# Optimization experiments

Hardware: AMD Instinct MI355X
Metric: run time of the kernel (lower is better)

The kernel has to match this reference:

```python
import jax, jax.numpy as jnp
import numpy as np


def _scattering(image, mags, phases):
    # image: [B,S,S] real; mags/phases: [J,L,S,S] real (Fourier-domain Morlet filters)
    J = mags.shape[0]
    psi = (mags * jnp.exp(1j * phases)).astype(jnp.complex64)        # [J,L,S,S]
    xf = jnp.fft.fft2(image)                                          # [B,S,S] complex64
    # first-order: modulus of wavelet convolutions, all scales/orientations at once
    u1 = jnp.abs(jnp.fft.ifft2(xf[:, None, None] * psi[None]))        # [B,J,L,S,S]
    s0 = image.mean(axis=(-2, -1))                                    # [B]
    s1 = u1.mean(axis=(2, 3, 4))                                      # [B,J] (orientation-averaged)
    # second-order: only j2 > j1 (the nan-filtered entries in the original)
    s2_parts = []
    for j1 in range(J - 1):  # structural loop over scales, not data dims
        u1f = jnp.fft.fft2(u1[:, j1].astype(jnp.complex64))           # [B,L1,S,S]
        psi2 = psi[j1 + 1:]                                           # [J2,L2,S,S]
        v = jnp.abs(jnp.fft.ifft2(u1f[:, :, None, None] * psi2[None, None]))  # [B,L1,J2,L2,S,S]
        s2_parts.append(v.mean(axis=(1, 3, 4, 5)))                    # [B,J2]
    s2 = jnp.concatenate(s2_parts, axis=1)                            # [B, J*(J-1)/2]
    return s0, s1, s2


def setup_inputs() -> dict:
    key = jax.random.key(0)
    ks = jax.random.split(key, 8)
    B, S, J, L = 64, 128, 6, 4
    return {
        "image_batch": jax.random.normal(ks[0], (B, S, S), dtype=jnp.float32),
        "mags": jax.random.uniform(ks[1], (J, L, S, S), dtype=jnp.float32),
        "phases": jax.random.normal(ks[2], (J, L, S, S), dtype=jnp.float32),
        "w1": jax.random.normal(ks[3], (22, 16), dtype=jnp.float32) * 0.1,
        "b1": jnp.zeros((16,), dtype=jnp.float32),
        "w2": jax.random.normal(ks[4], (16, 16), dtype=jnp.float32) * 0.1,
        "b2": jnp.zeros((16,), dtype=jnp.float32),
        "w3": jax.random.normal(ks[5], (16, 1), dtype=jnp.float32) * 0.1,
        "b3": jnp.zeros((1,), dtype=jnp.float32),
    }


def reference(image_batch, mags, phases, w1, b1, w2, b2, w3, b3):
    s0, s1, s2 = _scattering(image_batch, mags, phases)
    x = jnp.concatenate([s0[:, None], s1, s2], axis=1)                # [B,22]
    x = jax.nn.relu(x @ w1 + b1)
    x = jax.nn.relu(x @ w2 + b2)
    x = jax.nn.sigmoid(x @ w3 + b3)
    return jnp.squeeze(x, axis=1)                                     # [B]
```

## Files before the change

kernel.cpp:

```cpp
#include <hip/hip_runtime.h>
#include <math.h>


#define SDIM 128
#define PLANE 16384
#define PITCH 129
#define NT 1024
#define TWO_PI 6.28318530717958647692f

constexpr float W16R[8] = {1.f, 0.9238795325f, 0.7071067812f, 0.3826834324f,
                           0.f, -0.3826834324f, -0.7071067812f, -0.9238795325f};
constexpr float W16I[8] = {0.f, -0.3826834324f, -0.7071067812f, -0.9238795325f,
                           -1.f, -0.9238795325f, -0.7071067812f, -0.3826834324f};

__device__ __forceinline__ float fast_sqrtf(float x) {
  return __builtin_amdgcn_sqrtf(x);
}

__device__ __forceinline__ unsigned packbf(float re, float im) {
  const unsigned r = __float_as_uint(re) + 0x8000u;
  const unsigned i = __float_as_uint(im) + 0x8000u;
  return __builtin_amdgcn_perm(r, i, 0x07060302u);
}
__device__ __forceinline__ void unpackbf(unsigned u, float& re, float& im) {
  re = __uint_as_float(u & 0xFFFF0000u);
  im = __uint_as_float(u << 16);
}

__device__ __forceinline__ void stC(float2* s, int idx, float re, float im) { s[idx] = make_float2(re, im); }
__device__ __forceinline__ void ldC(const float2* s, int idx, float& re, float& im) { const float2 v = s[idx]; re = v.x; im = v.y; }
__device__ __forceinline__ void stC(unsigned* s, int idx, float re, float im) { s[idx] = packbf(re, im); }
__device__ __forceinline__ void ldC(const unsigned* s, int idx, float& re, float& im) { unpackbf(s[idx], re, im); }

__device__ __forceinline__ void load_tw(const float2* __restrict__ twg, int g,
                                        float* twr, float* twi) {
#pragma unroll
  for (int k = 1; k < 16; ++k) {
    const float2 w = twg[16 * g + k];
    twr[k] = __uint_as_float(__builtin_amdgcn_readfirstlane(__float_as_uint(w.x)));
    twi[k] = __uint_as_float(__builtin_amdgcn_readfirstlane(__float_as_uint(w.y)));
  }
}

template<bool INV>
__device__ __forceinline__ void bfly(float& ar, float& ai, float& br, float& bi, const int idx) {
  float tr, ti;
  if (idx == 0) {
    tr = br; ti = bi;
  } else if (idx == 4) {
    if (INV) { tr = -bi; ti = br; } else { tr = bi; ti = -br; }
  } else {
    const float wr = W16R[idx];
    const float wi = INV ? -W16I[idx] : W16I[idx];
    tr = br * wr - bi * wi;
    ti = br * wi + bi * wr;
  }
  br = ar - tr; bi = ai - ti;
  ar = ar + tr; ai = ai + ti;
}

#define CSWAP(re, im, a, b) { float _t = re[a]; re[a]=re[b]; re[b]=_t; _t = im[a]; im[a]=im[b]; im[b]=_t; }

template<bool INV>
__device__ __forceinline__ void dft16(float* re, float* im) {
  CSWAP(re, im, 1, 8) CSWAP(re, im, 2, 4) CSWAP(re, im, 3, 12)
  CSWAP(re, im, 5, 10) CSWAP(re, im, 7, 14) CSWAP(re, im, 11, 13)
#pragma unroll
  for (int ls = 1; ls <= 4; ++ls) {
    const int len = 1 << ls, half = len >> 1, tstep = 16 >> ls;
#pragma unroll
    for (int blk = 0; blk < 16; blk += len)
#pragma unroll
      for (int j = 0; j < half; ++j)
        bfly<INV>(re[blk + j], im[blk + j], re[blk + j + half], im[blk + j + half], j * tstep);
  }
}

template<bool INV>
__device__ __forceinline__ void dft8(float* re, float* im) {
  CSWAP(re, im, 1, 4) CSWAP(re, im, 3, 6)
#pragma unroll
  for (int ls = 1; ls <= 3; ++ls) {
    const int len = 1 << ls, half = len >> 1, tstep = 8 >> ls;
#pragma unroll
    for (int blk = 0; blk < 8; blk += len)
#pragma unroll
      for (int j = 0; j < half; ++j)
        bfly<INV>(re[blk + j], im[blk + j], re[blk + j + half], im[blk + j + half], j * tstep * 2);
  }
}

__device__ __forceinline__ void twmul_fwd(float* R, float* I, const float* twr, const float* twi) {
#pragma unroll
  for (int k = 1; k < 16; ++k) {
    const float r = R[k] * twr[k] - I[k] * twi[k];
    I[k] = R[k] * twi[k] + I[k] * twr[k]; R[k] = r;
  }
}
__device__ __forceinline__ void twmul_inv(float* R, float* I, const float* twr, const float* twi) {
#pragma unroll
  for (int k = 1; k < 16; ++k) {
    const float r = R[k] * twr[k] + I[k] * twi[k];
    I[k] = I[k] * twr[k] - R[k] * twi[k]; R[k] = r;
  }
}

template<typename S>
__device__ __forceinline__ void fwd_fft2(float* R, float* I, S* sC,
                                         int g, int q, const float* twr, const float* twi) {
  const int rb = q * PITCH;
  dft16<false>(R, I);
  twmul_fwd(R, I, twr, twi);
  __syncthreads();
#pragma unroll
  for (int k = 0; k < 16; ++k) stC(sC, rb + 8 * k + g, R[k], I[k]);
  __syncthreads();
#pragma unroll
  for (int t = 0; t < 8; ++t) {
    ldC(sC, rb + 16 * g + t, R[t], I[t]);
    ldC(sC, rb + 16 * g + 8 + t, R[8 + t], I[8 + t]);
  }
  dft8<false>(R, I); dft8<false>(R + 8, I + 8);
#pragma unroll
  for (int k2 = 0; k2 < 8; ++k2) {
    stC(sC, rb + 16 * g + k2, R[k2], I[k2]);
    stC(sC, rb + 16 * g + 8 + k2, R[8 + k2], I[8 + k2]);
  }
  __syncthreads();
#pragma unroll
  for (int m = 0; m < 16; ++m) ldC(sC, (g + 8 * m) * PITCH + q, R[m], I[m]);
  dft16<false>(R, I);
  twmul_fwd(R, I, twr, twi);
#pragma unroll
  for (int k = 0; k < 16; ++k) stC(sC, (8 * k + g) * PITCH + q, R[k], I[k]);
  __syncthreads();
#pragma unroll
  for (int u = 0; u < 8; ++u) {
    const int bp = (16 * g + 2 * u) * PITCH + q;
    ldC(sC, bp, R[2 * u], I[2 * u]);
    ldC(sC, bp + PITCH, R[2 * u + 1], I[2 * u + 1]);
  }
  dft8<false>(R, I); dft8<false>(R + 8, I + 8);
}

template<bool FIRST, typename S>
__device__ __forceinline__ void inv_fft2(float* R, float* I, S* sC,
                                         int g, int q, const float* twr, const float* twi) {
  const int rb = q * PITCH;
  dft8<true>(R, I); dft8<true>(R + 8, I + 8);
  if constexpr (!FIRST) __syncthreads();
#pragma unroll
  for (int t = 0; t < 16; ++t) stC(sC, rb + 16 * g + t, R[t], I[t]);
  __syncthreads();
#pragma unroll
  for (int k = 0; k < 16; ++k) ldC(sC, rb + 8 * k + g, R[k], I[k]);
  twmul_inv(R, I, twr, twi);
  dft16<true>(R, I);
#pragma unroll
  for (int m = 0; m < 16; ++m) stC(sC, rb + g + 8 * m, R[m], I[m]);
  __syncthreads();
#pragma unroll
  for (int u = 0; u < 8; ++u) {
    const int bp = (16 * g + 2 * u) * PITCH + q;
    ldC(sC, bp, R[2 * u], I[2 * u]);
    ldC(sC, bp + PITCH, R[2 * u + 1], I[2 * u + 1]);
  }
  dft8<true>(R, I); dft8<true>(R + 8, I + 8);
#pragma unroll
  for (int u = 0; u < 8; ++u) {
    const int bp = (16 * g + 2 * u) * PITCH + q;
    stC(sC, bp, R[2 * u], I[2 * u]);
    stC(sC, bp + PITCH, R[2 * u + 1], I[2 * u + 1]);
  }
  __syncthreads();
#pragma unroll
  for (int k = 0; k < 16; ++k) ldC(sC, (8 * k + g) * PITCH + q, R[k], I[k]);
  twmul_inv(R, I, twr, twi);
  dft16<true>(R, I);
}

__device__ __forceinline__ float block_reduce_sum(float v, float* red, int tid) {
#pragma unroll
  for (int o = 32; o > 0; o >>= 1) v += __shfl_down(v, o);
  __syncthreads();
  if ((tid & 63) == 0) red[tid >> 6] = v;
  __syncthreads();
  float t = 0.0f;
  if (tid == 0) {
#pragma unroll
    for (int w = 0; w < 16; ++w) t += red[w];
  }
  return t;
}

__global__ __launch_bounds__(256) void k_psi(const float* __restrict__ mags,
                                             const float* __restrict__ phases,
                                             float2* __restrict__ psi,
                                             float2* __restrict__ twg) {
  if (blockIdx.x == 0 && threadIdx.x < 128) {
    const int gg = threadIdx.x >> 4, k = threadIdx.x & 15;
    float sn, cs;
    __sincosf(-TWO_PI * (float)(gg * k) * (1.0f / 128.0f), &sn, &cs);
    twg[threadIdx.x] = make_float2(cs, sn);
  }
  const int gid = blockIdx.x * 256 + threadIdx.x;
  const int p = gid >> 14;
  const int rem = gid & (PLANE - 1);
  const int e = rem & 1;
  const int tt = (rem >> 1) & 1023;
  const int i = rem >> 11;
  const int j = 2 * i + e;
  const int g = tt >> 7, q = tt & 127;
  const int pr = 16 * g + j, pc = q;
  const int kr = (pr >> 3) + 16 * (pr & 7);
  const int kc = (pc >> 3) + 16 * (pc & 7);
  const int src = (p << 14) + kr * SDIM + kc;
  const float m = mags[src] * (1.0f / 16384.0f);
  float sn, cs;
  __sincosf(phases[src], &sn, &cs);
  psi[gid] = make_float2(m * cs, m * sn);
}

__global__ __launch_bounds__(NT) void k_img_fft(const float* __restrict__ img,
                                                float2* __restrict__ Xf,
                                                float* __restrict__ s0,
                                                const float2* __restrict__ twg) {
  __shared__ float2 sC[SDIM * PITCH];
  __shared__ float red[16];
  const int tid = threadIdx.x, b = blockIdx.x;
  const int g = __builtin_amdgcn_readfirstlane(tid >> 7);
  const int q = tid & 127;
  float twr[16], twi[16];
  load_tw(twg, g, twr, twi);
  const float* ip = img + b * PLANE;
  float sum = 0.0f;
#pragma unroll
  for (int kk = 0; kk < 16; ++kk) {
    const int e = tid + kk * NT;
    const float v = ip[e];
    sC[(e >> 7) * PITCH + (e & 127)] = make_float2(v, 0.0f);
    sum += v;
  }
  const float tot = block_reduce_sum(sum, red, tid);
  if (tid == 0) s0[b] = tot * (1.0f / 16384.0f);
  __syncthreads();
  float R[16], I[16];
#pragma unroll
  for (int m = 0; m < 16; ++m) { R[m] = sC[q * PITCH + g + 8 * m].x; I[m] = 0.0f; }
  fwd_fft2(R, I, sC, g, q, twr, twi);
  float4* x4 = (float4*)Xf + (size_t)b * 8192 + tid;
#pragma unroll
  for (int i = 0; i < 8; ++i)
    x4[i * 1024] = make_float4(R[2 * i], I[2 * i], R[2 * i + 1], I[2 * i + 1]);
}

__global__ __launch_bounds__(NT) void k_scat_a(const float2* __restrict__ Xf,
                                               const float2* __restrict__ psi,
                                               float* __restrict__ s1num,
                                               unsigned* __restrict__ Ubuf,
                                               const float2* __restrict__ twg) {
  __shared__ unsigned sU[SDIM * PITCH];
  __shared__ float red[16];
  const int tid = threadIdx.x;
  const int g = __builtin_amdgcn_readfirstlane(tid >> 7);
  const int q = tid & 127;
  float twr[16], twi[16];
  load_tw(twg, g, twr, twi);
  const int bid = blockIdx.x;
  float R[16], I[16];

  if (bid < 1280) {
    const int j1 = bid >> 8;
    const int b = (bid & 255) >> 2;
    const int l1 = bid & 3;
    const float4* x4 = (const float4*)Xf + (size_t)b * 8192 + tid;
    const float4* p4 = (const float4*)psi + (size_t)(j1 * 4 + l1) * 8192 + tid;
#pragma unroll
    for (int i = 0; i < 8; ++i) {
      const float4 x = x4[i * 1024], v = p4[i * 1024];
      R[2 * i]     = x.x * v.x - x.y * v.y;  I[2 * i]     = x.x * v.y + x.y * v.x;
      R[2 * i + 1] = x.z * v.z - x.w * v.w;  I[2 * i + 1] = x.z * v.w + x.w * v.z;
    }
    inv_fft2<true>(R, I, sU, g, q, twr, twi);
    float s1sum = 0.0f;
#pragma unroll
    for (int m = 0; m < 16; ++m) {
      const float a = fast_sqrtf(R[m] * R[m] + I[m] * I[m]);
      s1sum += a; R[m] = a; I[m] = 0.0f;
    }
    fwd_fft2(R, I, sU, g, q, twr, twi);
    uint4 ob[4];
    unsigned* obs = (unsigned*)ob;
#pragma unroll
    for (int j = 0; j < 16; ++j) obs[j] = packbf(R[j], I[j]);
    uint4* o4 = (uint4*)Ubuf + (size_t)((b * 5 + j1) * 4 + l1) * 4096 + tid;
#pragma unroll
    for (int i = 0; i < 4; ++i) o4[i * 1024] = ob[i];
    const float tot = block_reduce_sum(s1sum, red, tid);
    if (tid == 0) atomicAdd(&s1num[b * 6 + j1], tot);
  } else {
    const int idx = bid - 1280;
    const int b = idx >> 2, l = idx & 3;
    const float4* x4 = (const float4*)Xf + (size_t)b * 8192 + tid;
    const float4* p4 = (const float4*)psi + (size_t)(20 + l) * 8192 + tid;
#pragma unroll
    for (int i = 0; i < 8; ++i) {
      const float4 x = x4[i * 1024], v = p4[i * 1024];
      R[2 * i]     = x.x * v.x - x.y * v.y;  I[2 * i]     = x.x * v.y + x.y * v.x;
      R[2 * i + 1] = x.z * v.z - x.w * v.w;  I[2 * i + 1] = x.z * v.w + x.w * v.z;
    }
    inv_fft2<true>(R, I, sU, g, q, twr, twi);
    float s = 0.0f;
#pragma unroll
    for (int m = 0; m < 16; ++m) s += fast_sqrtf(R[m] * R[m] + I[m] * I[m]);
    const float tot = block_reduce_sum(s, red, tid);
    if (tid == 0) atomicAdd(&s1num[b * 6 + 5], tot);
  }
}

__global__ __launch_bounds__(NT) void k_scat_b(const float2* __restrict__ psi,
                                               const unsigned* __restrict__ Ubuf,
                                               float* __restrict__ s2num,
                                               const float2* __restrict__ twg) {
  __shared__ unsigned sU[SDIM * PITCH];
  __shared__ float red[16];
  const int tid = threadIdx.x;
  const int g = __builtin_amdgcn_readfirstlane(tid >> 7);
  const int q = tid & 127;
  float twr[16], twi[16];
  load_tw(twg, g, twr, twi);
  int t = blockIdx.x;
  const int l2 = t & 3; t >>= 2;
  const int pair = t % 15; t /= 15;
  const int l1 = t & 3;
  const int b = t >> 2;
  int j1 = 0, base = 0;
  if (pair >= 14)      { j1 = 4; base = 14; }
  else if (pair >= 12) { j1 = 3; base = 12; }
  else if (pair >= 9)  { j1 = 2; base = 9; }
  else if (pair >= 5)  { j1 = 1; base = 5; }
  const int j2 = j1 + 1 + (pair - base);
  float R[16], I[16];
  {
    const uint4* u4 = (const uint4*)Ubuf + (size_t)((b * 5 + j1) * 4 + l1) * 4096 + tid;
    uint4 ub[4];
#pragma unroll
    for (int i = 0; i < 4; ++i) ub[i] = u4[i * 1024];
    const unsigned* ubs = (const unsigned*)ub;
    const float4* p4 = (const float4*)psi + (size_t)(j2 * 4 + l2) * 8192 + tid;
#pragma unroll
    for (int i = 0; i < 8; ++i) {
      const float4 v = p4[i * 1024];
      float ur, ui;
      unpackbf(ubs[2 * i], ur, ui);
      R[2 * i] = ur * v.x - ui * v.y;      I[2 * i] = ur * v.y + ui * v.x;
      unpackbf(ubs[2 * i + 1], ur, ui);
      R[2 * i + 1] = ur * v.z - ui * v.w;  I[2 * i + 1] = ur * v.w + ui * v.z;
    }
  }
  inv_fft2<true>(R, I, sU, g, q, twr, twi);
  float vsum = 0.0f;
#pragma unroll
  for (int m = 0; m < 16; ++m) vsum += fast_sqrtf(R[m] * R[m] + I[m] * I[m]);
  const float tot = block_reduce_sum(vsum, red, tid);
  if (tid == 0) atomicAdd(&s2num[b * 15 + pair], tot);
}

__global__ __launch_bounds__(NT) void k_scat_mono(const float2* __restrict__ Xf,
                                                  const float2* __restrict__ psi,
                                                  float* __restrict__ s1num,
                                                  float* __restrict__ s2num,
                                                  const float2* __restrict__ twg) {
  __shared__ unsigned sU[SDIM * PITCH];
  __shared__ float red[16];
  const int tid = threadIdx.x;
  const int g = __builtin_amdgcn_readfirstlane(tid >> 7);
  const int q = tid & 127;
  float twr[16], twi[16];
  load_tw(twg, g, twr, twi);
  const int bid = blockIdx.x;
  float R[16], I[16];
  if (bid < 1280) {
    const int j1 = bid >> 8;
    const int b = (bid & 255) >> 2;
    const int l1 = bid & 3;
    const float4* x4 = (const float4*)Xf + (size_t)b * 8192 + tid;
    const float4* p4 = (const float4*)psi + (size_t)(j1 * 4 + l1) * 8192 + tid;
#pragma unroll
    for (int i = 0; i < 8; ++i) {
      const float4 x = x4[i * 1024], v = p4[i * 1024];
      R[2 * i]     = x.x * v.x - x.y * v.y;  I[2 * i]     = x.x * v.y + x.y * v.x;
      R[2 * i + 1] = x.z * v.z - x.w * v.w;  I[2 * i + 1] = x.z * v.w + x.w * v.z;
    }
    inv_fft2<true>(R, I, sU, g, q, twr, twi);
    float s1sum = 0.0f;
#pragma unroll
    for (int m = 0; m < 16; ++m) {
      const float a = fast_sqrtf(R[m] * R[m] + I[m] * I[m]);
      s1sum += a; R[m] = a; I[m] = 0.0f;
    }
    fwd_fft2(R, I, sU, g, q, twr, twi);
    float Ur[16], Ui[16];
#pragma unroll
    for (int k = 0; k < 16; ++k) { Ur[k] = R[k]; Ui[k] = I[k]; }
    {
      const float tot = block_reduce_sum(s1sum, red, tid);
      if (tid == 0) atomicAdd(&s1num[b * 6 + j1], tot);
    }
    const int pb = (j1 * (11 - j1)) >> 1;
    int plane = (j1 + 1) * 4;
#pragma unroll 1
    for (int j2 = j1 + 1; j2 <= 5; ++j2) {
      float vsum = 0.0f;
#pragma unroll 1
      for (int l2 = 0; l2 < 4; ++l2) {
        const float4* q4 = (const float4*)psi + (size_t)plane * 8192 + tid;
#pragma unroll
        for (int i = 0; i < 8; ++i) {
          const float4 v = q4[i * 1024];
          R[2 * i]     = Ur[2 * i] * v.x - Ui[2 * i] * v.y;
          I[2 * i]     = Ur[2 * i] * v.y + Ui[2 * i] * v.x;
          R[2 * i + 1] = Ur[2 * i + 1] * v.z - Ui[2 * i + 1] * v.w;
          I[2 * i + 1] = Ur[2 * i + 1] * v.w + Ui[2 * i + 1] * v.z;
        }
        inv_fft2<false>(R, I, sU, g, q, twr, twi);
#pragma unroll
        for (int m = 0; m < 16; ++m) vsum += fast_sqrtf(R[m] * R[m] + I[m] * I[m]);
        ++plane;
      }
      const float tot = block_reduce_sum(vsum, red, tid);
      if (tid == 0) atomicAdd(&s2num[b * 15 + pb + (j2 - j1 - 1)], tot);
    }
  } else {
    const int idx = bid - 1280;
    const int b = idx >> 2, l = idx & 3;
    const float4* x4 = (const float4*)Xf + (size_t)b * 8192 + tid;
    const float4* p4 = (const float4*)psi + (size_t)(20 + l) * 8192 + tid;
#pragma unroll
    for (int i = 0; i < 8; ++i) {
      const float4 x = x4[i * 1024], v = p4[i * 1024];
      R[2 * i]     = x.x * v.x - x.y * v.y;  I[2 * i]     = x.x * v.y + x.y * v.x;
      R[2 * i + 1] = x.z * v.z - x.w * v.w;  I[2 * i + 1] = x.z * v.w + x.w * v.z;
    }
    inv_fft2<true>(R, I, sU, g, q, twr, twi);
    float s = 0.0f;
#pragma unroll
    for (int m = 0; m < 16; ++m) s += fast_sqrtf(R[m] * R[m] + I[m] * I[m]);
    const float tot = block_reduce_sum(s, red, tid);
    if (tid == 0) atomicAdd(&s1num[b * 6 + 5], tot);
  }
}

__global__ __launch_bounds__(64) void k_final(const float* __restrict__ s0,
                                              const float* __restrict__ s1num,
                                              const float* __restrict__ s2num,
                                              const float* __restrict__ w1,
                                              const float* __restrict__ b1,
                                              const float* __restrict__ w2,
                                              const float* __restrict__ b2,
                                              const float* __restrict__ w3,
                                              const float* __restrict__ b3,
                                              float* __restrict__ out) {
  const int b = threadIdx.x;
  if (b >= 64) return;
  float x[22];
  x[0] = s0[b];
#pragma unroll
  for (int j = 0; j < 6; ++j) x[1 + j] = s1num[b * 6 + j] * (1.0f / (4.0f * 16384.0f));
#pragma unroll
  for (int p = 0; p < 15; ++p) x[7 + p] = s2num[b * 15 + p] * (1.0f / (16.0f * 16384.0f));
  float h1[16];
#pragma unroll
  for (int o = 0; o < 16; ++o) {
    float t = b1[o];
    for (int i = 0; i < 22; ++i) t += x[i] * w1[i * 16 + o];
    h1[o] = fmaxf(t, 0.0f);
  }
  float h2[16];
#pragma unroll
  for (int o = 0; o < 16; ++o) {
    float t = b2[o];
    for (int i = 0; i < 16; ++i) t += h1[i] * w2[i * 16 + o];
    h2[o] = fmaxf(t, 0.0f);
  }
  float t = b3[0];
#pragma unroll
  for (int i = 0; i < 16; ++i) t += h2[i] * w3[i];
  out[b] = 1.0f / (1.0f + expf(-t));
}

extern "C" void kernel_launch(void* const* d_in, const int* in_sizes, int n_in,
                              void* d_out, int out_size, void* d_ws, size_t ws_size,
                              hipStream_t stream) {
  (void)in_sizes; (void)n_in; (void)out_size;
  const float* image  = (const float*)d_in[0];
  const float* mags   = (const float*)d_in[1];
  const float* phases = (const float*)d_in[2];
  const float* w1 = (const float*)d_in[3];
  const float* b1 = (const float*)d_in[4];
  const float* w2 = (const float*)d_in[5];
  const float* b2 = (const float*)d_in[6];
  const float* w3 = (const float*)d_in[7];
  const float* b3 = (const float*)d_in[8];
  float* out = (float*)d_out;

  char* ws = (char*)d_ws;
  float2* psi = (float2*)ws;
  float2* Xf  = (float2*)(ws + 3145728);
  float*  s0  = (float*)(ws + 11534336);
  float*  s1n = s0 + 64;
  float*  s2n = s1n + 384;
  float2* twg = (float2*)(s2n + 960);
  unsigned* Ubuf = (unsigned*)(ws + 11542528);
  const size_t need = 11542528ull + 83886080ull;

  hipMemsetAsync(s1n, 0, (384 + 960) * sizeof(float), stream);
  k_psi<<<dim3(1536), dim3(256), 0, stream>>>(mags, phases, psi, twg);
  k_img_fft<<<dim3(64), dim3(NT), 0, stream>>>(image, Xf, s0, twg);
  if (ws_size >= need) {
    k_scat_a<<<dim3(1536), dim3(NT), 0, stream>>>(Xf, psi, s1n, Ubuf, twg);
    k_scat_b<<<dim3(15360), dim3(NT), 0, stream>>>(psi, Ubuf, s2n, twg);
  } else {
    k_scat_mono<<<dim3(1536), dim3(NT), 0, stream>>>(Xf, psi, s1n, s2n, twg);
  }
  k_final<<<dim3(1), dim3(64), 0, stream>>>(s0, s1n, s2n, w1, b1, w2, b2, w3, b3, out);
}
```

Before: 502.2 us.

## Restructure 2D FFT shared-memory layout to replace block barriers with wave-local fences

Remaps thread-to-data assignment (g = tid&7, q = tid>>3) so that each radix-16/8 sub-FFT exchange stays inside one wavefront. Several __syncthreads are replaced by s_waitcnt LDS fences, and a new blocked transpose layout (TBLK stride) leaves only one full barrier per transpose. Twiddles are cut to 9 entries, with factors 9..15 built by multiplying by w8, which lowers register pressure. The psi permutation and the launch bounds are updated to match. The intra-wave fences depend on lockstep wavefront execution, and the extra complex multiplies add ALU work.

```diff
diff --git a/kernel.cpp b/kernel.cpp
--- a/kernel.cpp
+++ b/kernel.cpp
@@ -4,8 +4,9 @@
 
 #define SDIM 128
 #define PLANE 16384
-#define PITCH 129
 #define NT 1024
+#define SSTR 136
+#define TBLK 1088
 #define TWO_PI 6.28318530717958647692f
 
 constexpr float W16R[8] = {1.f, 0.9238795325f, 0.7071067812f, 0.3826834324f,
@@ -17,6 +18,10 @@
   return __builtin_amdgcn_sqrtf(x);
 }
 
+__device__ __forceinline__ void ldsfence() {
+  asm volatile("s_waitcnt lgkmcnt(0)" ::: "memory");
+}
+
 __device__ __forceinline__ unsigned packbf(float re, float im) {
   const unsigned r = __float_as_uint(re) + 0x8000u;
   const unsigned i = __float_as_uint(im) + 0x8000u;
@@ -32,14 +37,22 @@
 __device__ __forceinline__ void stC(unsigned* s, int idx, float re, float im) { s[idx] = packbf(re, im); }
 __device__ __forceinline__ void ldC(const unsigned* s, int idx, float& re, float& im) { unpackbf(s[idx], re, im); }
 
-__device__ __forceinline__ void load_tw(const float2* __restrict__ twg, int g,
-                                        float* twr, float* twi) {
-#pragma unroll
-  for (int k = 1; k < 16; ++k) {
-    const float2 w = twg[16 * g + k];
-    twr[k] = __uint_as_float(__builtin_amdgcn_readfirstlane(__float_as_uint(w.x)));
-    twi[k] = __uint_as_float(__builtin_amdgcn_readfirstlane(__float_as_uint(w.y)));
-  }
+__device__ __forceinline__ void load_tw8(const float2* __restrict__ twg, int g,
+                                         float* twr, float* twi) {
+  const float4* t4 = (const float4*)(twg + 16 * g);
+  const float4 a = t4[0];
+  const float4 b = t4[1];
+  const float4 c = t4[2];
+  const float4 d = t4[3];
+  const float2 e8 = twg[16 * g + 8];
+  twr[1] = a.z; twi[1] = a.w;
+  twr[2] = b.x; twi[2] = b.y;
+  twr[3] = b.z; twi[3] = b.w;
+  twr[4] = c.x; twi[4] = c.y;
+  twr[5] = c.z; twi[5] = c.w;
+  twr[6] = d.x; twi[6] = d.y;
+  twr[7] = d.z; twi[7] = d.w;
+  twr[8] = e8.x; twi[8] = e8.y;
 }
 
 template<bool INV>
@@ -92,91 +105,125 @@
 
 __device__ __forceinline__ void twmul_fwd(float* R, float* I, const float* twr, const float* twi) {
 #pragma unroll
-  for (int k = 1; k < 16; ++k) {
+  for (int k = 1; k <= 8; ++k) {
     const float r = R[k] * twr[k] - I[k] * twi[k];
     I[k] = R[k] * twi[k] + I[k] * twr[k]; R[k] = r;
   }
+#pragma unroll
+  for (int k = 9; k < 16; ++k) {
+    const float r = R[k] * twr[k - 8] - I[k] * twi[k - 8];
+    const float i = R[k] * twi[k - 8] + I[k] * twr[k - 8];
+    R[k] = r * twr[8] - i * twi[8];
+    I[k] = r * twi[8] + i * twr[8];
+  }
 }
 __device__ __forceinline__ void twmul_inv(float* R, float* I, const float* twr, const float* twi) {
 #pragma unroll
-  for (int k = 1; k < 16; ++k) {
+  for (int k = 1; k <= 8; ++k) {
     const float r = R[k] * twr[k] + I[k] * twi[k];
     I[k] = I[k] * twr[k] - R[k] * twi[k]; R[k] = r;
   }
+#pragma unroll
+  for (int k = 9; k < 16; ++k) {
+    const float r = R[k] * twr[k - 8] + I[k] * twi[k - 8];
+    const float i = I[k] * twr[k - 8] - R[k] * twi[k - 8];
+    R[k] = r * twr[8] + i * twi[8];
+    I[k] = i * twr[8] - r * twi[8];
+  }
+}
+
+template<typename S>
+__device__ __forceinline__ void inv_fft2(float* R, float* I, S* sC,
+                                         const float* twr, const float* twi,
+                                         int g, int q) {
+  const int sb = q * SSTR;
+  const int qh = q & 7, W = q >> 3;
+  dft8<true>(R, I); dft8<true>(R + 8, I + 8);
+  ldsfence();
+#pragma unroll
+  for (int r = 0; r < 8; ++r) {
+    stC(sC, sb + g + 17 * r,     R[r],     I[r]);
+    stC(sC, sb + g + 8 + 17 * r, R[8 + r], I[8 + r]);
+  }
+  ldsfence();
+#pragma unroll
+  for (int k = 0; k < 16; ++k) ldC(sC, sb + 17 * g + k, R[k], I[k]);
+  twmul_inv(R, I, twr, twi);
+  dft16<true>(R, I);
+  __syncthreads();
+  {
+    const int tb = qh + 8 * g + 64 * W;
+#pragma unroll
+    for (int s = 0; s < 16; ++s) stC(sC, tb + TBLK * s, R[s], I[s]);
+  }
+  __syncthreads();
+  {
+    const int tb = g + 8 * qh + TBLK * W;
+#pragma unroll
+    for (int k2 = 0; k2 < 8; ++k2) {
+      ldC(sC, tb + 128 * k2,      R[k2],     I[k2]);
+      ldC(sC, tb + 128 * k2 + 64, R[8 + k2], I[8 + k2]);
+    }
+  }
+  dft8<true>(R, I); dft8<true>(R + 8, I + 8);
+  ldsfence();
+#pragma unroll
+  for (int r = 0; r < 8; ++r) {
+    stC(sC, sb + g + 17 * r,     R[r],     I[r]);
+    stC(sC, sb + g + 8 + 17 * r, R[8 + r], I[8 + r]);
+  }
+  ldsfence();
+#pragma unroll
+  for (int k = 0; k < 16; ++k) ldC(sC, sb + 17 * g + k, R[k], I[k]);
+  twmul_inv(R, I, twr, twi);
+  dft16<true>(R, I);
 }
 
 template<typename S>
 __device__ __forceinline__ void fwd_fft2(float* R, float* I, S* sC,
-                                         int g, int q, const float* twr, const float* twi) {
-  const int rb = q * PITCH;
+                                         const float* twr, const float* twi,
+                                         int g, int q) {
+  const int sb = q * SSTR;
+  const int qh = q & 7, W = q >> 3;
   dft16<false>(R, I);
   twmul_fwd(R, I, twr, twi);
-  __syncthreads();
-#pragma unroll
-  for (int k = 0; k < 16; ++k) stC(sC, rb + 8 * k + g, R[k], I[k]);
-  __syncthreads();
-#pragma unroll
-  for (int t = 0; t < 8; ++t) {
-    ldC(sC, rb + 16 * g + t, R[t], I[t]);
-    ldC(sC, rb + 16 * g + 8 + t, R[8 + t], I[8 + t]);
+  ldsfence();
+#pragma unroll
+  for (int k = 0; k < 16; ++k) stC(sC, sb + 17 * g + k, R[k], I[k]);
+  ldsfence();
+#pragma unroll
+  for (int r = 0; r < 8; ++r) {
+    ldC(sC, sb + g + 17 * r,     R[r],     I[r]);
+    ldC(sC, sb + g + 8 + 17 * r, R[8 + r], I[8 + r]);
   }
   dft8<false>(R, I); dft8<false>(R + 8, I + 8);
-#pragma unroll
-  for (int k2 = 0; k2 < 8; ++k2) {
-    stC(sC, rb + 16 * g + k2, R[k2], I[k2]);
-    stC(sC, rb + 16 * g + 8 + k2, R[8 + k2], I[8 + k2]);
-  }
-  __syncthreads();
-#pragma unroll
-  for (int m = 0; m < 16; ++m) ldC(sC, (g + 8 * m) * PITCH + q, R[m], I[m]);
+  ldsfence();
+  {
+    const int tb = g + 8 * qh + TBLK * W;
+#pragma unroll
+    for (int k2 = 0; k2 < 8; ++k2) {
+      stC(sC, tb + 128 * k2,      R[k2],     I[k2]);
+      stC(sC, tb + 128 * k2 + 64, R[8 + k2], I[8 + k2]);
+    }
+  }
+  __syncthreads();
+  {
+    const int tb = qh + 8 * g + 64 * W;
+#pragma unroll
+    for (int s = 0; s < 16; ++s) ldC(sC, tb + TBLK * s, R[s], I[s]);
+  }
   dft16<false>(R, I);
   twmul_fwd(R, I, twr, twi);
-#pragma unroll
-  for (int k = 0; k < 16; ++k) stC(sC, (8 * k + g) * PITCH + q, R[k], I[k]);
-  __syncthreads();
-#pragma unroll
-  for (int u = 0; u < 8; ++u) {
-    const int bp = (16 * g + 2 * u) * PITCH + q;
-    ldC(sC, bp, R[2 * u], I[2 * u]);
-    ldC(sC, bp + PITCH, R[2 * u + 1], I[2 * u + 1]);
+  ldsfence();
+#pragma unroll
+  for (int k = 0; k < 16; ++k) stC(sC, sb + 17 * g + k, R[k], I[k]);
+  ldsfence();
+#pragma unroll
+  for (int r = 0; r < 8; ++r) {
+    ldC(sC, sb + g + 17 * r,     R[r],     I[r]);
+    ldC(sC, sb + g + 8 + 17 * r, R[8 + r], I[8 + r]);
   }
   dft8<false>(R, I); dft8<false>(R + 8, I + 8);
-}
-
-template<bool FIRST, typename S>
-__device__ __forceinline__ void inv_fft2(float* R, float* I, S* sC,
-                                         int g, int q, const float* twr, const float* twi) {
-  const int rb = q * PITCH;
-  dft8<true>(R, I); dft8<true>(R + 8, I + 8);
-  if constexpr (!FIRST) __syncthreads();
-#pragma unroll
-  for (int t = 0; t < 16; ++t) stC(sC, rb + 16 * g + t, R[t], I[t]);
-  __syncthreads();
-#pragma unroll
-  for (int k = 0; k < 16; ++k) ldC(sC, rb + 8 * k + g, R[k], I[k]);
-  twmul_inv(R, I, twr, twi);
-  dft16<true>(R, I);
-#pragma unroll
-  for (int m = 0; m < 16; ++m) stC(sC, rb + g + 8 * m, R[m], I[m]);
-  __syncthreads();
-#pragma unroll
-  for (int u = 0; u < 8; ++u) {
-    const int bp = (16 * g + 2 * u) * PITCH + q;
-    ldC(sC, bp, R[2 * u], I[2 * u]);
-    ldC(sC, bp + PITCH, R[2 * u + 1], I[2 * u + 1]);
-  }
-  dft8<true>(R, I); dft8<true>(R + 8, I + 8);
-#pragma unroll
-  for (int u = 0; u < 8; ++u) {
-    const int bp = (16 * g + 2 * u) * PITCH + q;
-    stC(sC, bp, R[2 * u], I[2 * u]);
-    stC(sC, bp + PITCH, R[2 * u + 1], I[2 * u + 1]);
-  }
-  __syncthreads();
-#pragma unroll
-  for (int k = 0; k < 16; ++k) ldC(sC, (8 * k + g) * PITCH + q, R[k], I[k]);
-  twmul_inv(R, I, twr, twi);
-  dft16<true>(R, I);
 }
 
 __device__ __forceinline__ float block_reduce_sum(float v, float* red, int tid) {
@@ -210,10 +257,9 @@
   const int tt = (rem >> 1) & 1023;
   const int i = rem >> 11;
   const int j = 2 * i + e;
-  const int g = tt >> 7, q = tt & 127;
-  const int pr = 16 * g + j, pc = q;
-  const int kr = (pr >> 3) + 16 * (pr & 7);
-  const int kc = (pc >> 3) + 16 * (pc & 7);
+  const int g = tt & 7, q = tt >> 3;
+  const int kr = q;
+  const int kc = g + 8 * (j >> 3) + 16 * (j & 7);
   const int src = (p << 14) + kr * SDIM + kc;
   const float m = mags[src] * (1.0f / 16384.0f);
   float sn, cs;
@@ -225,47 +271,50 @@
                                                 float2* __restrict__ Xf,
                                                 float* __restrict__ s0,
                                                 const float2* __restrict__ twg) {
-  __shared__ float2 sC[SDIM * PITCH];
+  __shared__ float2 sC[128 * SSTR];
   __shared__ float red[16];
   const int tid = threadIdx.x, b = blockIdx.x;
-  const int g = __builtin_amdgcn_readfirstlane(tid >> 7);
-  const int q = tid & 127;
-  float twr[16], twi[16];
-  load_tw(twg, g, twr, twi);
+  const int g = tid & 7, q = tid >> 3;
+  float twr[9], twi[9];
+  load_tw8(twg, g, twr, twi);
   const float* ip = img + b * PLANE;
   float sum = 0.0f;
 #pragma unroll
   for (int kk = 0; kk < 16; ++kk) {
     const int e = tid + kk * NT;
     const float v = ip[e];
-    sC[(e >> 7) * PITCH + (e & 127)] = make_float2(v, 0.0f);
+    const int nr = e >> 7, nc = e & 127;
+    sC[(nr & 7) + 8 * (nc & 7) + 64 * (nr >> 3) + TBLK * (nc >> 3)] = make_float2(v, 0.0f);
     sum += v;
   }
   const float tot = block_reduce_sum(sum, red, tid);
   if (tid == 0) s0[b] = tot * (1.0f / 16384.0f);
   __syncthreads();
   float R[16], I[16];
-#pragma unroll
-  for (int m = 0; m < 16; ++m) { R[m] = sC[q * PITCH + g + 8 * m].x; I[m] = 0.0f; }
-  fwd_fft2(R, I, sC, g, q, twr, twi);
+  {
+    const int tb = g + 8 * (q & 7) + TBLK * (q >> 3);
+#pragma unroll
+    for (int s = 0; s < 16; ++s) { R[s] = sC[tb + 64 * s].x; I[s] = 0.0f; }
+  }
+  __syncthreads();
+  fwd_fft2(R, I, sC, twr, twi, g, q);
   float4* x4 = (float4*)Xf + (size_t)b * 8192 + tid;
 #pragma unroll
   for (int i = 0; i < 8; ++i)
     x4[i * 1024] = make_float4(R[2 * i], I[2 * i], R[2 * i + 1], I[2 * i + 1]);
 }
 
-__global__ __launch_bounds__(NT) void k_scat_a(const float2* __restrict__ Xf,
-                                               const float2* __restrict__ psi,
-                                               float* __restrict__ s1num,
-                                               unsigned* __restrict__ Ubuf,
-                                               const float2* __restrict__ twg) {
-  __shared__ unsigned sU[SDIM * PITCH];
+__global__ __launch_bounds__(NT, 8) void k_scat_a(const float2* __restrict__ Xf,
+                                                  const float2* __restrict__ psi,
+                                                  float* __restrict__ s1num,
+                                                  unsigned* __restrict__ Ubuf,
+                                                  const float2* __restrict__ twg) {
+  __shared__ unsigned sU[128 * SSTR];
   __shared__ float red[16];
   const int tid = threadIdx.x;
-  const int g = __builtin_amdgcn_readfirstlane(tid >> 7);
-  const int q = tid & 127;
-  float twr[16], twi[16];
-  load_tw(twg, g, twr, twi);
+  const int g = tid & 7, q = tid >> 3;
+  float twr[9], twi[9];
+  load_tw8(twg, g, twr, twi);
   const int bid = blockIdx.x;
   float R[16], I[16];
 
@@ -281,14 +330,14 @@
       R[2 * i]     = x.x * v.x - x.y * v.y;  I[2 * i]     = x.x * v.y + x.y * v.x;
       R[2 * i + 1] = x.z * v.z - x.w * v.w;  I[2 * i + 1] = x.z * v.w + x.w * v.z;
     }
-    inv_fft2<true>(R, I, sU, g, q, twr, twi);
+    inv_fft2(R, I, sU, twr, twi, g, q);
     float s1sum = 0.0f;
 #pragma unroll
     for (int m = 0; m < 16; ++m) {
       const float a = fast_sqrtf(R[m] * R[m] + I[m] * I[m]);
       s1sum += a; R[m] = a; I[m] = 0.0f;
     }
-    fwd_fft2(R, I, sU, g, q, twr, twi);
+    fwd_fft2(R, I, sU, twr, twi, g, q);
     uint4 ob[4];
     unsigned* obs = (unsigned*)ob;
 #pragma unroll
@@ -309,7 +358,7 @@
       R[2 * i]     = x.x * v.x - x.y * v.y;  I[2 * i]     = x.x * v.y + x.y * v.x;
       R[2 * i + 1] = x.z * v.z - x.w * v.w;  I[2 * i + 1] = x.z * v.w + x.w * v.z;
     }
-    inv_fft2<true>(R, I, sU, g, q, twr, twi);
+    inv_fft2(R, I, sU, twr, twi, g, q);
     float s = 0.0f;
 #pragma unroll
     for (int m = 0; m < 16; ++m) s += fast_sqrtf(R[m] * R[m] + I[m] * I[m]);
@@ -318,17 +367,16 @@
   }
 }
 
-__global__ __launch_bounds__(NT) void k_scat_b(const float2* __restrict__ psi,
-                                               const unsigned* __restrict__ Ubuf,
-                                               float* __restrict__ s2num,
-                                               const float2* __restrict__ twg) {
-  __shared__ unsigned sU[SDIM * PITCH];
+__global__ __launch_bounds__(NT, 8) void k_scat_b(const float2* __restrict__ psi,
+                                                  const unsigned* __restrict__ Ubuf,
+                                                  float* __restrict__ s2num,
+                                                  const float2* __restrict__ twg) {
+  __shared__ unsigned sU[128 * SSTR];
   __shared__ float red[16];
   const int tid = threadIdx.x;
-  const int g = __builtin_amdgcn_readfirstlane(tid >> 7);
-  const int q = tid & 127;
-  float twr[16], twi[16];
-  load_tw(twg, g, twr, twi);
+  const int g = tid & 7, q = tid >> 3;
+  float twr[9], twi[9];
+  load_tw8(twg, g, twr, twi);
   int t = blockIdx.x;
   const int l2 = t & 3; t >>= 2;
   const int pair = t % 15; t /= 15;
@@ -358,7 +406,7 @@
       R[2 * i + 1] = ur * v.z - ui * v.w;  I[2 * i + 1] = ur * v.w + ui * v.z;
     }
   }
-  inv_fft2<true>(R, I, sU, g, q, twr, twi);
+  inv_fft2(R, I, sU, twr, twi, g, q);
   float vsum = 0.0f;
 #pragma unroll
   for (int m = 0; m < 16; ++m) vsum += fast_sqrtf(R[m] * R[m] + I[m] * I[m]);
@@ -371,13 +419,12 @@
                                                   float* __restrict__ s1num,
                                                   float* __restrict__ s2num,
                                                   const float2* __restrict__ twg) {
-  __shared__ unsigned sU[SDIM * PITCH];
+  __shared__ unsigned sU[128 * SSTR];
   __shared__ float red[16];
   const int tid = threadIdx.x;
-  const int g = __builtin_amdgcn_readfirstlane(tid >> 7);
-  const int q = tid & 127;
-  float twr[16], twi[16];
-  load_tw(twg, g, twr, twi);
+  const int g = tid & 7, q = tid >> 3;
+  float twr[9], twi[9];
+  load_tw8(twg, g, twr, twi);
   const int bid = blockIdx.x;
   float R[16], I[16];
   if (bid < 1280) {
@@ -392,14 +439,14 @@
       R[2 * i]     = x.x * v.x - x.y * v.y;  I[2 * i]     = x.x * v.y + x.y * v.x;
       R[2 * i + 1] = x.z * v.z - x.w * v.w;  I[2 * i + 1] = x.z * v.w + x.w * v.z;
     }
-    inv_fft2<true>(R, I, sU, g, q, twr, twi);
+    inv_fft2(R, I, sU, twr, twi, g, q);
     float s1sum = 0.0f;
 #pragma unroll
     for (int m = 0; m < 16; ++m) {
       const float a = fast_sqrtf(R[m] * R[m] + I[m] * I[m]);
       s1sum += a; R[m] = a; I[m] = 0.0f;
     }
-    fwd_fft2(R, I, sU, g, q, twr, twi);
+    fwd_fft2(R, I, sU, twr, twi, g, q);
     float Ur[16], Ui[16];
 #pragma unroll
     for (int k = 0; k < 16; ++k) { Ur[k] = R[k]; Ui[k] = I[k]; }
@@ -423,7 +470,7 @@
           R[2 * i + 1] = Ur[2 * i + 1] * v.z - Ui[2 * i + 1] * v.w;
           I[2 * i + 1] = Ur[2 * i + 1] * v.w + Ui[2 * i + 1] * v.z;
         }
-        inv_fft2<false>(R, I, sU, g, q, twr, twi);
+        inv_fft2(R, I, sU, twr, twi, g, q);
 #pragma unroll
         for (int m = 0; m < 16; ++m) vsum += fast_sqrtf(R[m] * R[m] + I[m] * I[m]);
         ++plane;
@@ -442,7 +489,7 @@
       R[2 * i]     = x.x * v.x - x.y * v.y;  I[2 * i]     = x.x * v.y + x.y * v.x;
       R[2 * i + 1] = x.z * v.z - x.w * v.w;  I[2 * i + 1] = x.z * v.w + x.w * v.z;
     }
-    inv_fft2<true>(R, I, sU, g, q, twr, twi);
+    inv_fft2(R, I, sU, twr, twi, g, q);
     float s = 0.0f;
 #pragma unroll
     for (int m = 0; m < 16; ++m) s += fast_sqrtf(R[m] * R[m] + I[m] * I[m]);
```

Measured after the change: 593.4 us. +18.2%, slower.

## Run second-order inverse FFTs in packed fp16 with two filters per thread

Applied to the files above, without the earlier changes.

Adds a half-precision second-order kernel that packs two orientation filters into h2 vectors. Each block computes two inverse 2D FFTs with packed fp16 arithmetic, which halves the block count. A scaled fp16 copy of the filters and the twiddles is precomputed in the psi kernel, and the final kernel undoes the scale. This trades accuracy, through fp16 rounding and range limits in the FFT butterflies, for halved ALU work per filter, and it uses a larger shared tile of uint2.

```diff
diff --git a/kernel.cpp b/kernel.cpp
--- a/kernel.cpp
+++ b/kernel.cpp
@@ -7,15 +7,16 @@
 #define PITCH 129
 #define NT 1024
 #define TWO_PI 6.28318530717958647692f
+#define PSIH_SCALE 16.0f
+
+typedef _Float16 h2 __attribute__((ext_vector_type(2)));
 
 constexpr float W16R[8] = {1.f, 0.9238795325f, 0.7071067812f, 0.3826834324f,
                            0.f, -0.3826834324f, -0.7071067812f, -0.9238795325f};
 constexpr float W16I[8] = {0.f, -0.3826834324f, -0.7071067812f, -0.9238795325f,
                            -1.f, -0.9238795325f, -0.7071067812f, -0.3826834324f};
 
-__device__ __forceinline__ float fast_sqrtf(float x) {
-  return __builtin_amdgcn_sqrtf(x);
-}
+__device__ __forceinline__ float fast_sqrtf(float x) { return __builtin_amdgcn_sqrtf(x); }
 
 __device__ __forceinline__ unsigned packbf(float re, float im) {
   const unsigned r = __float_as_uint(re) + 0x8000u;
@@ -27,6 +28,11 @@
   im = __uint_as_float(u << 16);
 }
 
+union UHU { unsigned u; h2 h; };
+__device__ __forceinline__ h2 u2h(unsigned u) { UHU x; x.u = u; return x.h; }
+__device__ __forceinline__ unsigned h2u(h2 h) { UHU x; x.h = h; return x.u; }
+__device__ __forceinline__ h2 bch2(float f) { const _Float16 h = (_Float16)f; h2 v = {h, h}; return v; }
+
 __device__ __forceinline__ void stC(float2* s, int idx, float re, float im) { s[idx] = make_float2(re, im); }
 __device__ __forceinline__ void ldC(const float2* s, int idx, float& re, float& im) { const float2 v = s[idx]; re = v.x; im = v.y; }
 __device__ __forceinline__ void stC(unsigned* s, int idx, float re, float im) { s[idx] = packbf(re, im); }
@@ -41,13 +47,21 @@
     twi[k] = __uint_as_float(__builtin_amdgcn_readfirstlane(__float_as_uint(w.y)));
   }
 }
+__device__ __forceinline__ void load_twh(const uint2* __restrict__ twgh, int g,
+                                         unsigned* twru, unsigned* twiu) {
+#pragma unroll
+  for (int k = 1; k < 16; ++k) {
+    const uint2 w = twgh[16 * g + k];
+    twru[k] = (unsigned)__builtin_amdgcn_readfirstlane((int)w.x);
+    twiu[k] = (unsigned)__builtin_amdgcn_readfirstlane((int)w.y);
+  }
+}
 
 template<bool INV>
 __device__ __forceinline__ void bfly(float& ar, float& ai, float& br, float& bi, const int idx) {
   float tr, ti;
-  if (idx == 0) {
-    tr = br; ti = bi;
-  } else if (idx == 4) {
+  if (idx == 0) { tr = br; ti = bi; }
+  else if (idx == 4) {
     if (INV) { tr = -bi; ti = br; } else { tr = bi; ti = -br; }
   } else {
     const float wr = W16R[idx];
@@ -179,6 +193,94 @@
   dft16<true>(R, I);
 }
 
+__device__ __forceinline__ void bfly_h_inv(h2& ar, h2& ai, h2& br, h2& bi, const int idx) {
+  h2 tr, ti;
+  if (idx == 0) { tr = br; ti = bi; }
+  else if (idx == 4) { tr = -bi; ti = br; }
+  else {
+    const h2 wr = bch2(W16R[idx]);
+    const h2 wi = bch2(-W16I[idx]);
+    tr = br * wr - bi * wi;
+    ti = br * wi + bi * wr;
+  }
+  br = ar - tr; bi = ai - ti;
+  ar = ar + tr; ai = ai + ti;
+}
+
+#define HSWAP(re, im, a, b) { h2 _t = re[a]; re[a]=re[b]; re[b]=_t; _t = im[a]; im[a]=im[b]; im[b]=_t; }
+
+__device__ __forceinline__ void dft16h(h2* re, h2* im) {
+  HSWAP(re, im, 1, 8) HSWAP(re, im, 2, 4) HSWAP(re, im, 3, 12)
+  HSWAP(re, im, 5, 10) HSWAP(re, im, 7, 14) HSWAP(re, im, 11, 13)
+#pragma unroll
+  for (int ls = 1; ls <= 4; ++ls) {
+    const int len = 1 << ls, half = len >> 1, tstep = 16 >> ls;
+#pragma unroll
+    for (int blk = 0; blk < 16; blk += len)
+#pragma unroll
+      for (int j = 0; j < half; ++j)
+        bfly_h_inv(re[blk + j], im[blk + j], re[blk + j + half], im[blk + j + half], j * tstep);
+  }
+}
+
+__device__ __forceinline__ void dft8h(h2* re, h2* im) {
+  HSWAP(re, im, 1, 4) HSWAP(re, im, 3, 6)
+#pragma unroll
+  for (int ls = 1; ls <= 3; ++ls) {
+    const int len = 1 << ls, half = len >> 1, tstep = 8 >> ls;
+#pragma unroll
+    for (int blk = 0; blk < 8; blk += len)
+#pragma unroll
+      for (int j = 0; j < half; ++j)
+        bfly_h_inv(re[blk + j], im[blk + j], re[blk + j + half], im[blk + j + half], j * tstep * 2);
+  }
+}
+
+__device__ __forceinline__ void twmul_inv_h(h2* R, h2* I, const unsigned* twru, const unsigned* twiu) {
+#pragma unroll
+  for (int k = 1; k < 16; ++k) {
+    const h2 wr = u2h(twru[k]), wi = u2h(twiu[k]);
+    const h2 r = R[k] * wr + I[k] * wi;
+    I[k] = I[k] * wr - R[k] * wi;
+    R[k] = r;
+  }
+}
+
+__device__ __forceinline__ void inv_fft2_h(h2* R, h2* I, uint2* sC,
+                                           int g, int q,
+                                           const unsigned* twru, const unsigned* twiu) {
+  const int rb = q * PITCH;
+  dft8h(R, I); dft8h(R + 8, I + 8);
+#pragma unroll
+  for (int t = 0; t < 16; ++t) sC[rb + 16 * g + t] = make_uint2(h2u(R[t]), h2u(I[t]));
+  __syncthreads();
+#pragma unroll
+  for (int k = 0; k < 16; ++k) { const uint2 v = sC[rb + 8 * k + g]; R[k] = u2h(v.x); I[k] = u2h(v.y); }
+  twmul_inv_h(R, I, twru, twiu);
+  dft16h(R, I);
+#pragma unroll
+  for (int m = 0; m < 16; ++m) sC[rb + g + 8 * m] = make_uint2(h2u(R[m]), h2u(I[m]));
+  __syncthreads();
+#pragma unroll
+  for (int u = 0; u < 8; ++u) {
+    const int bp = (16 * g + 2 * u) * PITCH + q;
+    const uint2 v0 = sC[bp];         R[2 * u] = u2h(v0.x);     I[2 * u] = u2h(v0.y);
+    const uint2 v1 = sC[bp + PITCH]; R[2 * u + 1] = u2h(v1.x); I[2 * u + 1] = u2h(v1.y);
+  }
+  dft8h(R, I); dft8h(R + 8, I + 8);
+#pragma unroll
+  for (int u = 0; u < 8; ++u) {
+    const int bp = (16 * g + 2 * u) * PITCH + q;
+    sC[bp]         = make_uint2(h2u(R[2 * u]),     h2u(I[2 * u]));
+    sC[bp + PITCH] = make_uint2(h2u(R[2 * u + 1]), h2u(I[2 * u + 1]));
+  }
+  __syncthreads();
+#pragma unroll
+  for (int k = 0; k < 16; ++k) { const uint2 v = sC[(8 * k + g) * PITCH + q]; R[k] = u2h(v.x); I[k] = u2h(v.y); }
+  twmul_inv_h(R, I, twru, twiu);
+  dft16h(R, I);
+}
+
 __device__ __forceinline__ float block_reduce_sum(float v, float* red, int tid) {
 #pragma unroll
   for (int o = 32; o > 0; o >>= 1) v += __shfl_down(v, o);
@@ -196,29 +298,61 @@
 __global__ __launch_bounds__(256) void k_psi(const float* __restrict__ mags,
                                              const float* __restrict__ phases,
                                              float2* __restrict__ psi,
-                                             float2* __restrict__ twg) {
+                                             float2* __restrict__ twg,
+                                             uint2* __restrict__ psih2,
+                                             uint2* __restrict__ twgh) {
   if (blockIdx.x == 0 && threadIdx.x < 128) {
     const int gg = threadIdx.x >> 4, k = threadIdx.x & 15;
     float sn, cs;
     __sincosf(-TWO_PI * (float)(gg * k) * (1.0f / 128.0f), &sn, &cs);
     twg[threadIdx.x] = make_float2(cs, sn);
+    twgh[threadIdx.x] = make_uint2(h2u(bch2(cs)), h2u(bch2(sn)));
   }
   const int gid = blockIdx.x * 256 + threadIdx.x;
-  const int p = gid >> 14;
-  const int rem = gid & (PLANE - 1);
-  const int e = rem & 1;
-  const int tt = (rem >> 1) & 1023;
-  const int i = rem >> 11;
-  const int j = 2 * i + e;
-  const int g = tt >> 7, q = tt & 127;
-  const int pr = 16 * g + j, pc = q;
-  const int kr = (pr >> 3) + 16 * (pr & 7);
-  const int kc = (pc >> 3) + 16 * (pc & 7);
-  const int src = (p << 14) + kr * SDIM + kc;
-  const float m = mags[src] * (1.0f / 16384.0f);
-  float sn, cs;
-  __sincosf(phases[src], &sn, &cs);
-  psi[gid] = make_float2(m * cs, m * sn);
+  if (gid < 24 * PLANE) {
+    const int p = gid >> 14;
+    const int rem = gid & (PLANE - 1);
+    const int e = rem & 1;
+    const int tt = (rem >> 1) & 1023;
+    const int i = rem >> 11;
+    const int j = 2 * i + e;
+    const int g = tt >> 7, q = tt & 127;
+    const int pr = 16 * g + j, pc = q;
+    const int kr = (pr >> 3) + 16 * (pr & 7);
+    const int kc = (pc >> 3) + 16 * (pc & 7);
+    const int src = (p << 14) + kr * SDIM + kc;
+    const float m = mags[src] * (1.0f / 16384.0f);
+    float sn, cs;
+    __sincosf(phases[src], &sn, &cs);
+    psi[gid] = make_float2(m * cs, m * sn);
+  } else if (gid < 24 * PLANE + 10 * PLANE) {
+    const int c = gid - 24 * PLANE;
+    const int jp = c >> 14;
+    const int c14 = c & (PLANE - 1);
+    const int e2 = c14 & 1;
+    const int tmp = c14 >> 1;
+    const int tt = tmp & 1023;
+    const int i = tmp >> 10;
+    const int j = 2 * i + e2;
+    const int g = tt >> 7, q = tt & 127;
+    const int pr = 16 * g + j, pc = q;
+    const int kr = (pr >> 3) + 16 * (pr & 7);
+    const int kc = (pc >> 3) + 16 * (pc & 7);
+    const int j2 = 1 + (jp >> 1);
+    const int epair = jp & 1;
+    const int plane_lo = j2 * 4 + 2 * epair;
+    const int src_lo = (plane_lo << 14) + kr * SDIM + kc;
+    const int src_hi = src_lo + PLANE;
+    const float scl = PSIH_SCALE / 16384.0f;
+    const float m0 = mags[src_lo] * scl;
+    const float m1 = mags[src_hi] * scl;
+    float sn0, cs0, sn1, cs1;
+    __sincosf(phases[src_lo], &sn0, &cs0);
+    __sincosf(phases[src_hi], &sn1, &cs1);
+    h2 re2 = { (_Float16)(m0 * cs0), (_Float16)(m1 * cs1) };
+    h2 im2 = { (_Float16)(m0 * sn0), (_Float16)(m1 * sn1) };
+    psih2[(jp << 14) + c14] = make_uint2(h2u(re2), h2u(im2));
+  }
 }
 
 __global__ __launch_bounds__(NT) void k_img_fft(const float* __restrict__ img,
@@ -316,6 +450,70 @@
     const float tot = block_reduce_sum(s, red, tid);
     if (tid == 0) atomicAdd(&s1num[b * 6 + 5], tot);
   }
+}
+
+__global__ __launch_bounds__(NT) void k_scat_b_h2(const uint4* __restrict__ psih4,
+                                                  const unsigned* __restrict__ Ubuf,
+                                                  float* __restrict__ s2num,
+                                                  const uint2* __restrict__ twgh) {
+  __shared__ uint2 sU[SDIM * PITCH];
+  __shared__ float red[16];
+  const int tid = threadIdx.x;
+  const int g = __builtin_amdgcn_readfirstlane(tid >> 7);
+  const int q = tid & 127;
+  unsigned twru[16], twiu[16];
+  load_twh(twgh, g, twru, twiu);
+  int t = blockIdx.x;
+  const int e = t & 1; t >>= 1;
+  const int l1 = t & 3; t >>= 2;
+  const int pair = t % 15;
+  const int b = t / 15;
+  int j1 = 0, base = 0;
+  if (pair >= 14)      { j1 = 4; base = 14; }
+  else if (pair >= 12) { j1 = 3; base = 12; }
+  else if (pair >= 9)  { j1 = 2; base = 9; }
+  else if (pair >= 5)  { j1 = 1; base = 5; }
+  const int j2 = j1 + 1 + (pair - base);
+  const int jp = (j2 - 1) * 2 + e;
+
+  h2 R2[16], I2[16];
+  {
+    const uint4* u4 = (const uint4*)Ubuf + (size_t)((b * 5 + j1) * 4 + l1) * 4096 + tid;
+    uint4 ub[4];
+#pragma unroll
+    for (int i = 0; i < 4; ++i) ub[i] = u4[i * 1024];
+    const unsigned* ubs = (const unsigned*)ub;
+    const uint4* p4 = psih4 + (size_t)jp * 8192 + tid;
+#pragma unroll
+    for (int i = 0; i < 8; ++i) {
+      const uint4 pv = p4[i * 1024];
+      float ur, ui;
+      unpackbf(ubs[2 * i], ur, ui);
+      {
+        const h2 UR = bch2(ur), UI = bch2(ui);
+        const h2 pr = u2h(pv.x), pi = u2h(pv.y);
+        R2[2 * i] = UR * pr - UI * pi;
+        I2[2 * i] = UR * pi + UI * pr;
+      }
+      unpackbf(ubs[2 * i + 1], ur, ui);
+      {
+        const h2 UR = bch2(ur), UI = bch2(ui);
+        const h2 pr = u2h(pv.z), pi = u2h(pv.w);
+        R2[2 * i + 1] = UR * pr - UI * pi;
+        I2[2 * i + 1] = UR * pi + UI * pr;
+      }
+    }
+  }
+  inv_fft2_h(R2, I2, sU, g, q, twru, twiu);
+  float vsum = 0.0f;
+#pragma unroll
+  for (int m = 0; m < 16; ++m) {
+    const float rl = (float)R2[m].x, il = (float)I2[m].x;
+    const float rh = (float)R2[m].y, ih = (float)I2[m].y;
+    vsum += fast_sqrtf(rl * rl + il * il) + fast_sqrtf(rh * rh + ih * ih);
+  }
+  const float tot = block_reduce_sum(vsum, red, tid);
+  if (tid == 0) atomicAdd(&s2num[b * 15 + pair], tot);
 }
 
 __global__ __launch_bounds__(NT) void k_scat_b(const float2* __restrict__ psi,
@@ -460,7 +658,8 @@
                                               const float* __restrict__ b2,
                                               const float* __restrict__ w3,
                                               const float* __restrict__ b3,
-                                              float* __restrict__ out) {
+                                              float* __restrict__ out,
+                                              float s2scale) {
   const int b = threadIdx.x;
   if (b >= 64) return;
   float x[22];
@@ -468,7 +667,7 @@
 #pragma unroll
   for (int j = 0; j < 6; ++j) x[1 + j] = s1num[b * 6 + j] * (1.0f / (4.0f * 16384.0f));
 #pragma unroll
-  for (int p = 0; p < 15; ++p) x[7 + p] = s2num[b * 15 + p] * (1.0f / (16.0f * 16384.0f));
+  for (int p = 0; p < 15; ++p) x[7 + p] = s2num[b * 15 + p] * s2scale;
   float h1[16];
 #pragma unroll
   for (int o = 0; o < 16; ++o) {
@@ -476,16 +675,16 @@
     for (int i = 0; i < 22; ++i) t += x[i] * w1[i * 16 + o];
     h1[o] = fmaxf(t, 0.0f);
   }
-  float h2[16];
+  float h2a[16];
 #pragma unroll
   for (int o = 0; o < 16; ++o) {
     float t = b2[o];
     for (int i = 0; i < 16; ++i) t += h1[i] * w2[i * 16 + o];
-    h2[o] = fmaxf(t, 0.0f);
+    h2a[o] = fmaxf(t, 0.0f);
   }
   float t = b3[0];
 #pragma unroll
-  for (int i = 0; i < 16; ++i) t += h2[i] * w3[i];
+  for (int i = 0; i < 16; ++i) t += h2a[i] * w3[i];
   out[b] = 1.0f / (1.0f + expf(-t));
 }
 
@@ -511,17 +710,32 @@
   float*  s1n = s0 + 64;
   float*  s2n = s1n + 384;
   float2* twg = (float2*)(s2n + 960);
+  uint2*  twgh = (uint2*)((char*)twg + 1024);
   unsigned* Ubuf = (unsigned*)(ws + 11542528);
-  const size_t need = 11542528ull + 83886080ull;
+  uint2*  psih2 = (uint2*)(ws + 95428608);
+  const size_t need_r5 = 11542528ull + 83886080ull;
+  const size_t need_h2 = need_r5 + 1310720ull;
 
   hipMemsetAsync(s1n, 0, (384 + 960) * sizeof(float), stream);
-  k_psi<<<dim3(1536), dim3(256), 0, stream>>>(mags, phases, psi, twg);
-  k_img_fft<<<dim3(64), dim3(NT), 0, stream>>>(image, Xf, s0, twg);
-  if (ws_size >= need) {
+  if (ws_size >= need_h2) {
+    k_psi<<<dim3(2176), dim3(256), 0, stream>>>(mags, phases, psi, twg, psih2, twgh);
+    k_img_fft<<<dim3(64), dim3(NT), 0, stream>>>(image, Xf, s0, twg);
+    k_scat_a<<<dim3(1536), dim3(NT), 0, stream>>>(Xf, psi, s1n, Ubuf, twg);
+    k_scat_b_h2<<<dim3(7680), dim3(NT), 0, stream>>>((const uint4*)psih2, Ubuf, s2n, twgh);
+    k_final<<<dim3(1), dim3(64), 0, stream>>>(s0, s1n, s2n, w1, b1, w2, b2, w3, b3, out,
+                                              1.0f / (16.0f * 16384.0f * PSIH_SCALE));
+  } else if (ws_size >= need_r5) {
+    k_psi<<<dim3(1536), dim3(256), 0, stream>>>(mags, phases, psi, twg, psih2, twgh);
+    k_img_fft<<<dim3(64), dim3(NT), 0, stream>>>(image, Xf, s0, twg);
     k_scat_a<<<dim3(1536), dim3(NT), 0, stream>>>(Xf, psi, s1n, Ubuf, twg);
     k_scat_b<<<dim3(15360), dim3(NT), 0, stream>>>(psi, Ubuf, s2n, twg);
+    k_final<<<dim3(1), dim3(64), 0, stream>>>(s0, s1n, s2n, w1, b1, w2, b2, w3, b3, out,
+                                              1.0f / (16.0f * 16384.0f));
   } else {
+    k_psi<<<dim3(1536), dim3(256), 0, stream>>>(mags, phases, psi, twg, psih2, twgh);
+    k_img_fft<<<dim3(64), dim3(NT), 0, stream>>>(image, Xf, s0, twg);
     k_scat_mono<<<dim3(1536), dim3(NT), 0, stream>>>(Xf, psi, s1n, s2n, twg);
-  }
-  k_final<<<dim3(1), dim3(64), 0, stream>>>(s0, s1n, s2n, w1, b1, w2, b2, w3, b3, out);
-}
+    k_final<<<dim3(1), dim3(64), 0, stream>>>(s0, s1n, s2n, w1, b1, w2, b2, w3, b3, out,
+                                              1.0f / (16.0f * 16384.0f));
+  }
+}
```

After: 482.3 us. -4.0%, faster.
